# Kernel optimization log

Measured on AMD Instinct MI355X. Metric: run time of the kernel, lower is better.

The kernel has to match this reference:

```python
import jax, jax.numpy as jnp
import numpy as np

NUM_PIECE_TYPES = 7
NUM_COLORS = 3
NUM_CASTLING_STATES = 16
NUM_EP_STATES = 9
D = 256
B = 4096
EPS = 1e-5


def setup_inputs() -> dict:
    key = jax.random.key(0)
    ks = jax.random.split(key, 12)
    inp = {
        'piece_ids': jax.random.randint(ks[0], (B, 64), 0, NUM_PIECE_TYPES),
        'color_ids': jax.random.randint(ks[1], (B, 64), 0, NUM_COLORS),
        'turn': jax.random.randint(ks[2], (B,), 0, 2),
        'castling': jax.random.randint(ks[3], (B,), 0, NUM_CASTLING_STATES),
        'ep_file': jax.random.randint(ks[4], (B,), 0, NUM_EP_STATES),
        # learned parameters
        'piece_table': jax.random.normal(ks[5], (NUM_PIECE_TYPES, D), jnp.float32) * 0.02,
        'W': jax.random.normal(ks[6], (NUM_COLORS, D, D), jnp.float32) * (1.0 / np.sqrt(D)),
        'b': jax.random.normal(ks[7], (NUM_COLORS, D), jnp.float32) * 0.02,
        'square_table': jax.random.normal(ks[8], (64, D), jnp.float32) * 0.02,
        'turn_table': jax.random.normal(ks[9], (2, D), jnp.float32) * 0.02,
        'castling_table': jax.random.normal(ks[10], (NUM_CASTLING_STATES, D), jnp.float32) * 0.02,
        'ep_table': jax.random.normal(ks[11], (NUM_EP_STATES, D), jnp.float32) * 0.02,
        'gamma': jnp.ones((D,), jnp.float32),
        'beta': jnp.zeros((D,), jnp.float32),
    }
    return inp


def _layernorm(x, gamma, beta):
    mu = jnp.mean(x, axis=-1, keepdims=True)
    var = jnp.mean(jnp.square(x - mu), axis=-1, keepdims=True)
    return (x - mu) * jax.lax.rsqrt(var + EPS) * gamma + beta


def reference(piece_ids, color_ids, turn, castling, ep_file,
              piece_table, W, b, square_table, turn_table,
              castling_table, ep_table, gamma, beta):
    piece_emb = piece_table[piece_ids]                      # (B,64,D)
    # per-color linear: proj_stack[b,s,c] = piece_emb[b,s] @ W[c].T + b[c]
    proj_stack = jnp.einsum('bsd,cod->bsco', piece_emb, W) + b  # (B,64,C,D)
    # select the projection for each square's color (== one-hot mask + sum)
    idx = color_ids[..., None, None]                        # (B,64,1,1)
    sq_emb = jnp.take_along_axis(proj_stack, idx, axis=2)[:, :, 0, :]  # (B,64,D)
    sq_emb = sq_emb + square_table[None, :, :]              # add positional
    turn_tok = turn_table[turn][:, None, :]                 # (B,1,D)
    castle_tok = castling_table[castling][:, None, :]       # (B,1,D)
    ep_tok = ep_table[ep_file][:, None, :]                  # (B,1,D)
    tokens = jnp.concatenate([turn_tok, castle_tok, ep_tok, sq_emb], axis=1)  # (B,67,D)
    return _layernorm(tokens, gamma, beta)
```

## Files before the change

kernel.cpp:

```cpp
#include <hip/hip_runtime.h>


#define DIM 256
#define NPT 7
#define NCOL 3
#define NROWS_SQ (NPT * NCOL * 64)
#define ROW_TURN 1344
#define ROW_CASTLE 1346
#define ROW_EP 1362
#define NROWS_TOT 1371
#define EPSV 1e-5f

__device__ __forceinline__ float4 ln4(float4 x, float4 g, float4 bb) {
    float s = x.x + x.y + x.z + x.w;
    #pragma unroll
    for (int m = 1; m < 64; m <<= 1) s += __shfl_xor(s, m, 64);
    float mu = s * (1.0f / DIM);
    float dx = x.x - mu, dy = x.y - mu, dz = x.z - mu, dw = x.w - mu;
    float v = dx * dx + dy * dy + dz * dz + dw * dw;
    #pragma unroll
    for (int m = 1; m < 64; m <<= 1) v += __shfl_xor(v, m, 64);
    float inv = rsqrtf(v * (1.0f / DIM) + EPSV);
    return make_float4(dx * inv * g.x + bb.x,
                       dy * inv * g.y + bb.y,
                       dz * inv * g.z + bb.z,
                       dw * inv * g.w + bb.w);
}

__global__ __launch_bounds__(256) void table_kernel(
        const float* __restrict__ piece_table,
        const float* __restrict__ W,
        const float* __restrict__ bvec,
        const float* __restrict__ square_table,
        const float* __restrict__ turn_table,
        const float* __restrict__ castling_table,
        const float* __restrict__ ep_table,
        const float* __restrict__ gamma,
        const float* __restrict__ beta,
        float* __restrict__ table) {
    int e = blockIdx.x;
    int tid = threadIdx.x;
    int wave = tid >> 6, lane = tid & 63;
    float4 g  = ((const float4*)gamma)[lane];
    float4 bb = ((const float4*)beta)[lane];

    if (e < NPT * NCOL) {
        int p = e / NCOL, c = e % NCOL;
        __shared__ float pt[DIM];
        __shared__ float projs[DIM];
        pt[tid] = piece_table[p * DIM + tid];
        __syncthreads();
        const float4* w4 = (const float4*)(W + (size_t)c * DIM * DIM + (size_t)tid * DIM);
        float acc = bvec[c * DIM + tid];
        #pragma unroll 8
        for (int k = 0; k < DIM / 4; ++k) {
            float4 w = w4[k];
            acc += w.x * pt[k * 4 + 0] + w.y * pt[k * 4 + 1]
                 + w.z * pt[k * 4 + 2] + w.w * pt[k * 4 + 3];
        }
        projs[tid] = acc;
        __syncthreads();

        float4 a = ((const float4*)projs)[lane];
        float* tbase = table + (size_t)(p * (NCOL * 64) + c * 64) * DIM;
        for (int s = wave; s < 64; s += 4) {
            float4 q = ((const float4*)(square_table + s * DIM))[lane];
            float4 x = make_float4(a.x + q.x, a.y + q.y, a.z + q.z, a.w + q.w);
            ((float4*)(tbase + (size_t)s * DIM))[lane] = ln4(x, g, bb);
        }
    } else {
        for (int w = wave; w < 27; w += 4) {
            float4 x;
            if (w < 2) {
                x = ((const float4*)(turn_table + w * DIM))[lane];
            } else if (w < 18) {
                x = ((const float4*)(castling_table + (w - 2) * DIM))[lane];
            } else {
                x = ((const float4*)(ep_table + (w - 18) * DIM))[lane];
            }
            ((float4*)(table + (size_t)(ROW_TURN + w) * DIM))[lane] = ln4(x, g, bb);
        }
    }
}

__global__ __launch_bounds__(256) void gather_kernel(
        const int* __restrict__ piece_ids,
        const int* __restrict__ color_ids,
        const int* __restrict__ turn,
        const int* __restrict__ castling,
        const int* __restrict__ ep_file,
        const float* __restrict__ table,
        float* __restrict__ out) {
    int b = blockIdx.x;
    __shared__ int rows[67];
    int tid = threadIdx.x;
    if (tid < 64) {
        int pid = piece_ids[b * 64 + tid];
        int cid = color_ids[b * 64 + tid];
        rows[3 + tid] = pid * (NCOL * 64) + cid * 64 + tid;
    } else if (tid == 64) {
        rows[0] = ROW_TURN + turn[b];
    } else if (tid == 65) {
        rows[1] = ROW_CASTLE + castling[b];
    } else if (tid == 66) {
        rows[2] = ROW_EP + ep_file[b];
    }
    __syncthreads();

    int wave = tid >> 6, lane = tid & 63;
    float4* outb = (float4*)(out + (size_t)b * 67 * DIM);
    #pragma unroll 4
    for (int t = wave; t < 67; t += 4) {
        float4 v = ((const float4*)(table + (size_t)rows[t] * DIM))[lane];
        outb[t * (DIM / 4) + lane] = v;
    }
}

extern "C" void kernel_launch(void* const* d_in, const int* in_sizes, int n_in,
                              void* d_out, int out_size, void* d_ws, size_t ws_size,
                              hipStream_t stream) {
    const int*   piece_ids      = (const int*)d_in[0];
    const int*   color_ids      = (const int*)d_in[1];
    const int*   turn           = (const int*)d_in[2];
    const int*   castling       = (const int*)d_in[3];
    const int*   ep_file        = (const int*)d_in[4];
    const float* piece_table    = (const float*)d_in[5];
    const float* W              = (const float*)d_in[6];
    const float* bvec           = (const float*)d_in[7];
    const float* square_table   = (const float*)d_in[8];
    const float* turn_table     = (const float*)d_in[9];
    const float* castling_table = (const float*)d_in[10];
    const float* ep_table       = (const float*)d_in[11];
    const float* gamma          = (const float*)d_in[12];
    const float* beta           = (const float*)d_in[13];
    float* out = (float*)d_out;

    int B = in_sizes[0] / 64;
    float* table = (float*)d_ws;

    table_kernel<<<NPT * NCOL + 1, 256, 0, stream>>>(
        piece_table, W, bvec, square_table, turn_table, castling_table,
        ep_table, gamma, beta, table);
    gather_kernel<<<B, 256, 0, stream>>>(
        piece_ids, color_ids, turn, castling, ep_file, table, out);
}
```

Before: 74.73 us.

## Fuse table build and gather into one cooperative kernel with grid sync

Merges the table-building and gather kernels into a single cooperative launch of 512 blocks. Blocks build the normalized lookup table, meet at a grid-wide barrier, then copy output rows in a grid-stride loop using nontemporal stores. The aim is to remove the second launch and the gap between kernels, and to keep the large output write from polluting cache. The cost is the grid sync overhead, only 22 blocks doing table work while the rest wait, and per-row index loads that are no longer shared through LDS.

```diff
diff --git a/kernel.cpp b/kernel.cpp
--- a/kernel.cpp
+++ b/kernel.cpp
@@ -1,4 +1,7 @@
 #include <hip/hip_runtime.h>
+#include <hip/hip_cooperative_groups.h>
+
+namespace cg = cooperative_groups;
 
 
 #define DIM 256
@@ -10,6 +13,9 @@
 #define ROW_EP 1362
 #define NROWS_TOT 1371
 #define EPSV 1e-5f
+#define COOP_GRID 512
+
+typedef float f32x4 __attribute__((ext_vector_type(4)));
 
 __device__ __forceinline__ float4 ln4(float4 x, float4 g, float4 bb) {
     float s = x.x + x.y + x.z + x.w;
@@ -27,7 +33,8 @@
                        dw * inv * g.w + bb.w);
 }
 
-__global__ __launch_bounds__(256) void table_kernel(
+__device__ __forceinline__ void build_table_block(
+        int e, int tid, int wave, int lane,
         const float* __restrict__ piece_table,
         const float* __restrict__ W,
         const float* __restrict__ bvec,
@@ -38,12 +45,6 @@
         const float* __restrict__ gamma,
         const float* __restrict__ beta,
         float* __restrict__ table) {
-    int e = blockIdx.x;
-    int tid = threadIdx.x;
-    int wave = tid >> 6, lane = tid & 63;
-    float4 g  = ((const float4*)gamma)[lane];
-    float4 bb = ((const float4*)beta)[lane];
-
     if (e < NPT * NCOL) {
         int p = e / NCOL, c = e % NCOL;
         __shared__ float pt[DIM];
@@ -61,6 +62,8 @@
         projs[tid] = acc;
         __syncthreads();
 
+        float4 g  = ((const float4*)gamma)[lane];
+        float4 bb = ((const float4*)beta)[lane];
         float4 a = ((const float4*)projs)[lane];
         float* tbase = table + (size_t)(p * (NCOL * 64) + c * 64) * DIM;
         for (int s = wave; s < 64; s += 4) {
@@ -68,7 +71,9 @@
             float4 x = make_float4(a.x + q.x, a.y + q.y, a.z + q.z, a.w + q.w);
             ((float4*)(tbase + (size_t)s * DIM))[lane] = ln4(x, g, bb);
         }
-    } else {
+    } else if (e == NPT * NCOL) {
+        float4 g  = ((const float4*)gamma)[lane];
+        float4 bb = ((const float4*)beta)[lane];
         for (int w = wave; w < 27; w += 4) {
             float4 x;
             if (w < 2) {
@@ -83,37 +88,85 @@
     }
 }
 
-__global__ __launch_bounds__(256) void gather_kernel(
+__device__ __forceinline__ int row_of(
+        int r, const int* __restrict__ piece_ids, const int* __restrict__ color_ids,
+        const int* __restrict__ turn, const int* __restrict__ castling,
+        const int* __restrict__ ep_file) {
+    int b = r / 67;
+    int t = r - b * 67;
+    if (t == 0) return ROW_TURN + turn[b];
+    if (t == 1) return ROW_CASTLE + castling[b];
+    if (t == 2) return ROW_EP + ep_file[b];
+    int s = t - 3;
+    int idx = b * 64 + s;
+    return piece_ids[idx] * (NCOL * 64) + color_ids[idx] * 64 + s;
+}
+
+__global__ __launch_bounds__(256) void fused_kernel(
         const int* __restrict__ piece_ids,
         const int* __restrict__ color_ids,
         const int* __restrict__ turn,
         const int* __restrict__ castling,
         const int* __restrict__ ep_file,
-        const float* __restrict__ table,
-        float* __restrict__ out) {
-    int b = blockIdx.x;
-    __shared__ int rows[67];
+        const float* __restrict__ piece_table,
+        const float* __restrict__ W,
+        const float* __restrict__ bvec,
+        const float* __restrict__ square_table,
+        const float* __restrict__ turn_table,
+        const float* __restrict__ castling_table,
+        const float* __restrict__ ep_table,
+        const float* __restrict__ gamma,
+        const float* __restrict__ beta,
+        float* __restrict__ table,
+        float* __restrict__ out,
+        int nrows) {
+    int e = blockIdx.x;
     int tid = threadIdx.x;
-    if (tid < 64) {
-        int pid = piece_ids[b * 64 + tid];
-        int cid = color_ids[b * 64 + tid];
-        rows[3 + tid] = pid * (NCOL * 64) + cid * 64 + tid;
-    } else if (tid == 64) {
-        rows[0] = ROW_TURN + turn[b];
-    } else if (tid == 65) {
-        rows[1] = ROW_CASTLE + castling[b];
-    } else if (tid == 66) {
-        rows[2] = ROW_EP + ep_file[b];
+    int wave = tid >> 6, lane = tid & 63;
+
+    build_table_block(e, tid, wave, lane, piece_table, W, bvec, square_table,
+                      turn_table, castling_table, ep_table, gamma, beta, table);
+
+    cg::this_grid().sync();
+
+    int stride = gridDim.x * 4;
+    for (int r = e * 4 + wave; r < nrows; r += stride) {
+        int row = row_of(r, piece_ids, color_ids, turn, castling, ep_file);
+        f32x4 v = ((const f32x4*)(table + (size_t)row * DIM))[lane];
+        __builtin_nontemporal_store(v, (f32x4*)(out + (size_t)r * DIM) + lane);
     }
-    __syncthreads();
-
-    int wave = tid >> 6, lane = tid & 63;
-    float4* outb = (float4*)(out + (size_t)b * 67 * DIM);
-    #pragma unroll 4
-    for (int t = wave; t < 67; t += 4) {
-        float4 v = ((const float4*)(table + (size_t)rows[t] * DIM))[lane];
-        outb[t * (DIM / 4) + lane] = v;
-    }
+}
+
+__global__ __launch_bounds__(256) void table_kernel(
+        const float* __restrict__ piece_table,
+        const float* __restrict__ W,
+        const float* __restrict__ bvec,
+        const float* __restrict__ square_table,
+        const float* __restrict__ turn_table,
+        const float* __restrict__ castling_table,
+        const float* __restrict__ ep_table,
+        const float* __restrict__ gamma,
+        const float* __restrict__ beta,
+        float* __restrict__ table) {
+    build_table_block(blockIdx.x, threadIdx.x, threadIdx.x >> 6, threadIdx.x & 63,
+                      piece_table, W, bvec, square_table, turn_table,
+                      castling_table, ep_table, gamma, beta, table);
+}
+
+__global__ void gather_kernel(const int* __restrict__ piece_ids,
+                              const int* __restrict__ color_ids,
+                              const int* __restrict__ turn,
+                              const int* __restrict__ castling,
+                              const int* __restrict__ ep_file,
+                              const float* __restrict__ table,
+                              float* __restrict__ out,
+                              int nrows) {
+    int r = blockIdx.x * 4 + (threadIdx.x >> 6);
+    if (r >= nrows) return;
+    int lane = threadIdx.x & 63;
+    int row = row_of(r, piece_ids, color_ids, turn, castling, ep_file);
+    f32x4 v = ((const f32x4*)(table + (size_t)row * DIM))[lane];
+    __builtin_nontemporal_store(v, (f32x4*)(out + (size_t)r * DIM) + lane);
 }
 
 extern "C" void kernel_launch(void* const* d_in, const int* in_sizes, int n_in,
@@ -136,11 +189,24 @@
     float* out = (float*)d_out;
 
     int B = in_sizes[0] / 64;
+    int nrows = B * 67;
     float* table = (float*)d_ws;
 
-    table_kernel<<<NPT * NCOL + 1, 256, 0, stream>>>(
-        piece_table, W, bvec, square_table, turn_table, castling_table,
-        ep_table, gamma, beta, table);
-    gather_kernel<<<B, 256, 0, stream>>>(
-        piece_ids, color_ids, turn, castling, ep_file, table, out);
-}
+    void* args[] = {
+        (void*)&piece_ids, (void*)&color_ids, (void*)&turn, (void*)&castling,
+        (void*)&ep_file, (void*)&piece_table, (void*)&W, (void*)&bvec,
+        (void*)&square_table, (void*)&turn_table, (void*)&castling_table,
+        (void*)&ep_table, (void*)&gamma, (void*)&beta,
+        (void*)&table, (void*)&out, (void*)&nrows,
+    };
+    hipError_t err = hipLaunchCooperativeKernel((const void*)fused_kernel,
+                                                dim3(COOP_GRID), dim3(256),
+                                                args, 0, stream);
+    if (err != hipSuccess) {
+        table_kernel<<<NPT * NCOL + 1, 256, 0, stream>>>(
+            piece_table, W, bvec, square_table, turn_table, castling_table,
+            ep_table, gamma, beta, table);
+        gather_kernel<<<(nrows + 3) / 4, 256, 0, stream>>>(
+            piece_ids, color_ids, turn, castling, ep_file, table, out, nrows);
+    }
+}
```

Measured after the change: 167.7 us. 124% more time.
